# Performance work log

Hardware: AMD Instinct MI355X
Metric: run time of the kernel (lower is better)

Reference implementation:

```python
import jax, jax.numpy as jnp
import numpy as np

NUM_NEURONS = 256
NUM_SAMPLES = 512
MAX_SPIKES = 32
N_STEPS = 32          # fixed RK4 steps per spike round (stands in for adaptive Tsit5)
ALPHA = 0.03
V_RESET = 1.0
T0 = 0.0


def setup_inputs() -> dict:
    key = jax.random.key(0)
    ks = jax.random.split(key, 7)
    input_current = jax.random.normal(ks[0], (NUM_NEURONS,), dtype=jnp.float32)
    # _build_w with network=all-False: uniform(minval=0.5), mask sets nothing
    w = jax.random.uniform(ks[1], (NUM_NEURONS, NUM_NEURONS), minval=0.5, maxval=1.0, dtype=jnp.float32)
    mu = jax.random.uniform(ks[2], (2,), minval=0.5, maxval=1.0, dtype=jnp.float32)
    v0 = jax.random.normal(ks[3], (NUM_NEURONS,), dtype=jnp.float32)
    i0 = jax.random.normal(ks[4], (NUM_NEURONS,), dtype=jnp.float32)
    # s0 = log(U) - alpha  (always < 0)
    s0 = (jnp.log(jax.random.uniform(ks[5], (NUM_SAMPLES, NUM_NEURONS), minval=1e-6, maxval=1.0)) - ALPHA).astype(jnp.float32)
    # pre-drawn stochastic resets, one per (spike round, sample, neuron)
    reset_s = (jnp.log(jax.random.uniform(ks[6], (MAX_SPIKES, NUM_SAMPLES, NUM_NEURONS), minval=1e-6, maxval=1.0)) - ALPHA).astype(jnp.float32)
    return dict(input_current=input_current, w=w, mu=mu, v0=v0, i0=i0, s0=s0, reset_s=reset_s, t1=2)


def _drift(y, ic, mu1, mu2):
    # y: [samples, neurons, 3] = (v, i, s)
    v, i = y[..., 0], y[..., 1]
    dv = mu1 * (i + ic - v)
    di = -mu2 * i
    ds = jax.nn.sigmoid(v)  # intensity_fn(v)
    return jnp.stack([dv, di, ds], axis=-1)


def reference(input_current, w, mu, v0, i0, s0, reset_s, t1):
    t1f = jnp.float32(t1)
    mu1, mu2 = mu[0], mu[1]
    ic = input_current  # constant-in-time input current, [neurons]

    y0 = jnp.concatenate([
        jnp.broadcast_to(v0, (NUM_SAMPLES, NUM_NEURONS))[..., None],
        jnp.broadcast_to(i0, (NUM_SAMPLES, NUM_NEURONS))[..., None],
        s0[..., None]], axis=-1)  # [samples, neurons, 3]

    def rk4(y, h):
        k1 = _drift(y, ic, mu1, mu2)
        k2 = _drift(y + 0.5 * h * k1, ic, mu1, mu2)
        k3 = _drift(y + 0.5 * h * k2, ic, mu1, mu2)
        k4 = _drift(y + h * k3, ic, mu1, mu2)
        return y + (h / 6.0) * (k1 + 2.0 * k2 + 2.0 * k3 + k4)

    def round_body(carry, reset_k):
        t0s, y_in = carry                      # t0s: [samples]
        dt = (t1f - t0s) / N_STEPS             # per-sample step size
        h = dt[:, None, None]

        def step(sc, _):
            t, y, done, tev, yev, emask = sc
            y_new = rk4(y, h)
            y_new = jnp.where(done[:, None, None], y, y_new)  # freeze after event
            s_prev, s_new = y[..., 2], y_new[..., 2]
            crossed = s_new > 0.0                              # cond_fn root: s crosses 0
            trig = crossed.any(axis=1) & (~done)
            idx = jnp.argmax(s_new, axis=1)                    # event neuron (first/largest crossing)
            sp = jnp.take_along_axis(s_prev, idx[:, None], 1)[:, 0]
            sn = jnp.take_along_axis(s_new, idx[:, None], 1)[:, 0]
            frac = jnp.clip(sp / (sp - sn + 1e-12), 0.0, 1.0)  # linear root estimate (Newton stand-in)
            t_c = t + frac * dt
            y_c = y + frac[:, None, None] * (y_new - y)
            tev = jnp.where(trig, t_c, tev)
            yev = jnp.where(trig[:, None, None], y_c, yev)
            emask = jnp.where(trig[:, None], crossed, emask)
            y = jnp.where(trig[:, None, None], y_c, y_new)
            done = done | trig
            return (t + dt, y, done, tev, yev, emask), None

        done0 = jnp.zeros((NUM_SAMPLES,), bool)
        tev0 = jnp.full((NUM_SAMPLES,), jnp.inf, jnp.float32)
        em0 = jnp.zeros((NUM_SAMPLES, NUM_NEURONS), bool)
        (_, yend, done, tev, yev, emask), _ = jax.lax.scan(
            step, (t0s, y_in, done0, tev0, y_in, em0), None, length=N_STEPS)

        tev = jnp.where(done, tev, t1f)                 # no event -> sol.ts[-1] = t1
        yev = jnp.where(done[:, None, None], yev, yend)

        # trans_fn: spike reset + synaptic jump w[event_idx]
        eidx = jnp.argmax(emask, axis=1)
        w_row = jnp.where(done[:, None], w[eidx], 0.0)  # zero if no event happened
        v_t = yev[..., 0] - jnp.where(emask, V_RESET, 0.0)
        i_t = yev[..., 1] + w_row
        s_t = jnp.minimum(jnp.where(emask, reset_k, yev[..., 2]), 0.0)
        y_next = jnp.stack([v_t, i_t, s_t], axis=-1)
        return (tev, y_next), (tev, yev, emask)

    t0s = jnp.full((NUM_SAMPLES,), T0, jnp.float32)
    _, (tevs, yevs, emasks) = jax.lax.scan(jax.checkpoint(round_body), (t0s, y0), reset_s)

    spike_times = jnp.transpose(tevs, (1, 0))            # [samples, max_spikes]
    spike_values = jnp.transpose(yevs, (1, 0, 2, 3))     # [samples, max_spikes, neurons, 3]
    spike_marks = jnp.transpose(emasks, (1, 0, 2))       # [samples, max_spikes, neurons]
    return spike_times, spike_values, spike_marks
```

## Files before the change

kernel.cpp:

```cpp
#include <hip/hip_runtime.h>
#include <math.h>

#define NN 256
#define NS 512
#define MS 32
#define NSTEP 32
#define VRESET 1.0f

__device__ __forceinline__ float sigf(float x) {
    float e = __expf(-x);
    return __builtin_amdgcn_rcpf(1.0f + e);
}

__global__ __launch_bounds__(256) void snn_kernel(
    const float* __restrict__ ic_g,
    const float* __restrict__ w,
    const float* __restrict__ mu,
    const float* __restrict__ v0,
    const float* __restrict__ i0,
    const float* __restrict__ s0,
    const float* __restrict__ reset_s,
    const int*   __restrict__ t1p,
    float* __restrict__ out)
{
    const int tid  = threadIdx.x;
    const int lane = tid & 63;
    const int wid  = tid >> 6;
    const int samp = blockIdx.x;
    const double m1d = (double)mu[0];
    const double m2d = (double)mu[1];
    const float t1f = (float)t1p[0];

    __shared__ int   s_any[2][4];
    __shared__ float s_bv[4], s_bsp[4];
    __shared__ int   s_bn[4];
    __shared__ int   s_eidx[4];

    float v  = v0[tid];
    float ii = i0[tid];
    float s  = s0[samp * NN + tid];
    const float ic = ic_g[tid];
    float t0 = 0.0f;

    float* times = out;
    float* vals  = out + (size_t)NS * MS;
    float* marks = out + (size_t)NS * MS * (1 + NN * 3);

    for (int r = 0; r < MS; ++r) {
        const float dt = (t1f - t0) / (float)NSTEP;
        float tev = t1f;
        float yev_v, yev_i, yev_s;
        bool  em = false;
        bool  done = false;

        if (dt != 0.0f) {
            const double hd = (double)dt;
            const double a  = hd * m1d;
            const double b  = hd * m2d;
            const double p2 = 1.0 - 0.5 * a, q2 = 0.5 * a, r2 = 0.5 * a;
            const double i2c = 1.0 - 0.5 * b;
            const double p3 = 1.0 - 0.5 * a * p2;
            const double q3 = 0.5 * a * (i2c - q2);
            const double r3 = 0.5 * a * (1.0 - r2);
            const double i3c = 1.0 - 0.5 * b * i2c;
            const double p4 = 1.0 - a * p3;
            const double q4 = a * (i3c - q3);
            const double r4 = a * (1.0 - r3);
            const double i4c = 1.0 - b * i3c;
            const double a6 = a / 6.0, b6 = b / 6.0;
            const float fR00 = (float)(1.0 - a6 * (1.0 + 2.0 * p2 + 2.0 * p3 + p4));
            const float fR01 = (float)(a6 * (1.0 + 2.0 * (i2c - q2) + 2.0 * (i3c - q3) + (i4c - q4)));
            const float fC0  = (float)(a6 * (1.0 + 2.0 * (1.0 - r2) + 2.0 * (1.0 - r3) + (1.0 - r4)));
            const float fR11 = (float)(1.0 - b6 * (1.0 + 2.0 * i2c + 2.0 * i3c + i4c));
            const float fp2 = (float)p2, fq2 = (float)q2;
            const float fp3 = (float)p3, fq3 = (float)q3;
            const float fp4 = (float)p4, fq4 = (float)q4;
            const float r2ic = (float)r2 * ic;
            const float r3ic = (float)r3 * ic;
            const float r4ic = (float)r4 * ic;
            const float c0ic = fC0 * ic;
            const float h6 = dt * (1.0f / 6.0f);

            float t = t0, tprev = t0;
            float vp = v, ip = ii, sp = s;

            for (int st = 0; st <= NSTEP; ++st) {
                if (st > 0) {
                    int anyflag = s_any[(st - 1) & 1][0] | s_any[(st - 1) & 1][1] |
                                  s_any[(st - 1) & 1][2] | s_any[(st - 1) & 1][3];
                    if (anyflag) {
                        float bv = s, bsp = sp;
                        int   bn = tid;
#pragma unroll
                        for (int off = 32; off >= 1; off >>= 1) {
                            float ov  = __shfl_xor(bv, off);
                            float osp = __shfl_xor(bsp, off);
                            int   on  = __shfl_xor(bn, off);
                            if (ov > bv || (ov == bv && on < bn)) { bv = ov; bsp = osp; bn = on; }
                        }
                        if (lane == 0) { s_bv[wid] = bv; s_bsp[wid] = bsp; s_bn[wid] = bn; }
                        __syncthreads();
                        bv = s_bv[0]; bsp = s_bsp[0]; bn = s_bn[0];
#pragma unroll
                        for (int wv = 1; wv < 4; ++wv) {
                            float ov = s_bv[wv], osp = s_bsp[wv];
                            int   on = s_bn[wv];
                            if (ov > bv || (ov == bv && on < bn)) { bv = ov; bsp = osp; bn = on; }
                        }
                        float frac = bsp / (bsp - bv + 1e-12f);
                        frac = fminf(fmaxf(frac, 0.0f), 1.0f);
                        tev = tprev + frac * dt;
                        yev_v = vp + frac * (v  - vp);
                        yev_i = ip + frac * (ii - ip);
                        yev_s = sp + frac * (s  - sp);
                        em = s > 0.0f;
                        v = yev_v; ii = yev_i; s = yev_s;
                        done = true;
                        break;
                    }
                }
                if (st == NSTEP) break;

                vp = v; ip = ii; sp = s; tprev = t;
                float a2 = fmaf(fp2, vp, fmaf(fq2, ip, r2ic));
                float a3 = fmaf(fp3, vp, fmaf(fq3, ip, r3ic));
                float a4 = fmaf(fp4, vp, fmaf(fq4, ip, r4ic));
                float k1 = sigf(vp);
                float k2 = sigf(a2);
                float k3 = sigf(a3);
                float k4 = sigf(a4);
                v  = fmaf(fR00, vp, fmaf(fR01, ip, c0ic));
                ii = fR11 * ip;
                float ts = fmaf(2.0f, k2, k1);
                ts = fmaf(2.0f, k3, ts);
                ts = ts + k4;
                s = fmaf(h6, ts, sp);

                unsigned long long bl = __ballot(s > 0.0f);
                if (lane == 0) s_any[st & 1][wid] = (bl != 0ull) ? 1 : 0;
                t = tprev + dt;
                __syncthreads();
            }
        }

        if (!done) {
            tev = t1f;
            yev_v = v; yev_i = ii; yev_s = s; em = false;
        }

        const int sr = samp * MS + r;
        if (tid == 0) times[sr] = tev;
        {
            float* p = vals + ((size_t)sr * NN + tid) * 3;
            p[0] = yev_v;
            p[1] = yev_i;
            p[2] = yev_s;
            marks[(size_t)sr * NN + tid] = em ? 1.0f : 0.0f;
        }

        if (done) {
            unsigned long long bm = __ballot(em);
            int cand = (bm != 0ull) ? (wid * 64 + (int)__builtin_ctzll(bm)) : (2 * NN);
            if (lane == 0) s_eidx[wid] = cand;
            __syncthreads();
            int eidx = s_eidx[0];
            eidx = (s_eidx[1] < eidx) ? s_eidx[1] : eidx;
            eidx = (s_eidx[2] < eidx) ? s_eidx[2] : eidx;
            eidx = (s_eidx[3] < eidx) ? s_eidx[3] : eidx;

            float wr = w[eidx * NN + tid];
            v  = yev_v - (em ? VRESET : 0.0f);
            ii = yev_i + wr;
            float sres = em ? reset_s[((size_t)r * NS + samp) * NN + tid] : yev_s;
            s = fminf(sres, 0.0f);
        } else {
            s = fminf(s, 0.0f);
        }
        t0 = tev;
    }
}

extern "C" void kernel_launch(void* const* d_in, const int* in_sizes, int n_in,
                              void* d_out, int out_size, void* d_ws, size_t ws_size,
                              hipStream_t stream) {
    const float* ic      = (const float*)d_in[0];
    const float* w       = (const float*)d_in[1];
    const float* mu      = (const float*)d_in[2];
    const float* v0      = (const float*)d_in[3];
    const float* i0      = (const float*)d_in[4];
    const float* s0      = (const float*)d_in[5];
    const float* reset_s = (const float*)d_in[6];
    const int*   t1p     = (const int*)d_in[7];
    float* out = (float*)d_out;

    snn_kernel<<<dim3(NS), dim3(256), 0, stream>>>(ic, w, mu, v0, i0, s0,
                                                   reset_s, t1p, out);
}
```

Measured before the change: 158.1 us.

## Replace per-step block barriers with wave-local early exit and shared history

Removes the __syncthreads after every RK4 step. Each wave now integrates on its own, writes its s value per step into a shared history buffer, and on a local spike publishes the step via atomicMin and stops. Other waves poll the shared stop value. After a single barrier the block picks the earliest crossing step, reads s from history, and recomputes v and i by replaying the linear recurrence up to that step. The reset_s load is prefetched and the event-index reduction is merged into the argmax barrier. In exchange it adds about 33 KB of shared memory per block, which may cut occupancy, plus redundant replay work.

```diff
diff --git a/kernel.cpp b/kernel.cpp
--- a/kernel.cpp
+++ b/kernel.cpp
@@ -31,10 +31,10 @@
     const double m2d = (double)mu[1];
     const float t1f = (float)t1p[0];
 
-    __shared__ int   s_any[2][4];
+    __shared__ float s_hist[NSTEP + 1][NN];
+    __shared__ int   s_stop;
     __shared__ float s_bv[4], s_bsp[4];
-    __shared__ int   s_bn[4];
-    __shared__ int   s_eidx[4];
+    __shared__ int   s_bn[4], s_eidx[4];
 
     float v  = v0[tid];
     float ii = i0[tid];
@@ -52,6 +52,8 @@
         float yev_v, yev_i, yev_s;
         bool  em = false;
         bool  done = false;
+
+        const float rs_pref = reset_s[((size_t)r * NS + samp) * NN + tid];
 
         if (dt != 0.0f) {
             const double hd = (double)dt;
@@ -81,71 +83,102 @@
             const float c0ic = fC0 * ic;
             const float h6 = dt * (1.0f / 6.0f);
 
-            float t = t0, tprev = t0;
-            float vp = v, ip = ii, sp = s;
-
-            for (int st = 0; st <= NSTEP; ++st) {
-                if (st > 0) {
-                    int anyflag = s_any[(st - 1) & 1][0] | s_any[(st - 1) & 1][1] |
-                                  s_any[(st - 1) & 1][2] | s_any[(st - 1) & 1][3];
-                    if (anyflag) {
-                        float bv = s, bsp = sp;
-                        int   bn = tid;
-#pragma unroll
-                        for (int off = 32; off >= 1; off >>= 1) {
-                            float ov  = __shfl_xor(bv, off);
-                            float osp = __shfl_xor(bsp, off);
-                            int   on  = __shfl_xor(bn, off);
-                            if (ov > bv || (ov == bv && on < bn)) { bv = ov; bsp = osp; bn = on; }
-                        }
-                        if (lane == 0) { s_bv[wid] = bv; s_bsp[wid] = bsp; s_bn[wid] = bn; }
-                        __syncthreads();
-                        bv = s_bv[0]; bsp = s_bsp[0]; bn = s_bn[0];
-#pragma unroll
-                        for (int wv = 1; wv < 4; ++wv) {
-                            float ov = s_bv[wv], osp = s_bsp[wv];
-                            int   on = s_bn[wv];
-                            if (ov > bv || (ov == bv && on < bn)) { bv = ov; bsp = osp; bn = on; }
-                        }
-                        float frac = bsp / (bsp - bv + 1e-12f);
-                        frac = fminf(fmaxf(frac, 0.0f), 1.0f);
-                        tev = tprev + frac * dt;
-                        yev_v = vp + frac * (v  - vp);
-                        yev_i = ip + frac * (ii - ip);
-                        yev_s = sp + frac * (s  - sp);
-                        em = s > 0.0f;
-                        v = yev_v; ii = yev_i; s = yev_s;
-                        done = true;
-                        break;
-                    }
-                }
-                if (st == NSTEP) break;
-
-                vp = v; ip = ii; sp = s; tprev = t;
-                float a2 = fmaf(fp2, vp, fmaf(fq2, ip, r2ic));
-                float a3 = fmaf(fp3, vp, fmaf(fq3, ip, r3ic));
-                float a4 = fmaf(fp4, vp, fmaf(fq4, ip, r4ic));
-                float k1 = sigf(vp);
+            if (tid == 0) s_stop = NSTEP + 1;
+            s_hist[0][tid] = s;
+            __syncthreads();
+
+            float vv = v, iv = ii, sv = s;
+            int seen = NSTEP + 1;
+            for (int k = 1; k <= NSTEP; ++k) {
+                float a2 = fmaf(fp2, vv, fmaf(fq2, iv, r2ic));
+                float a3 = fmaf(fp3, vv, fmaf(fq3, iv, r3ic));
+                float a4 = fmaf(fp4, vv, fmaf(fq4, iv, r4ic));
+                float k1 = sigf(vv);
                 float k2 = sigf(a2);
                 float k3 = sigf(a3);
                 float k4 = sigf(a4);
-                v  = fmaf(fR00, vp, fmaf(fR01, ip, c0ic));
-                ii = fR11 * ip;
+                float vn  = fmaf(fR00, vv, fmaf(fR01, iv, c0ic));
+                float in_ = fR11 * iv;
                 float ts = fmaf(2.0f, k2, k1);
                 ts = fmaf(2.0f, k3, ts);
                 ts = ts + k4;
-                s = fmaf(h6, ts, sp);
-
-                unsigned long long bl = __ballot(s > 0.0f);
-                if (lane == 0) s_any[st & 1][wid] = (bl != 0ull) ? 1 : 0;
-                t = tprev + dt;
+                sv = fmaf(h6, ts, sv);
+                vv = vn; iv = in_;
+                s_hist[k][tid] = sv;
+                if (__any(sv > 0.0f)) {
+                    if (lane == 0) atomicMin(&s_stop, k);
+                    break;
+                }
+                if (seen <= k) break;
+                seen = *(volatile int*)&s_stop;
+            }
+            __syncthreads();
+            const int st = s_stop;
+
+            if (st <= NSTEP) {
+                float sn_ = s_hist[st][tid];
+                float sp_ = s_hist[st - 1][tid];
+                em = sn_ > 0.0f;
+
+                float bv = sn_, bsp = sp_;
+                int   bn = tid;
+#pragma unroll
+                for (int off = 32; off >= 1; off >>= 1) {
+                    float ov  = __shfl_xor(bv, off);
+                    float osp = __shfl_xor(bsp, off);
+                    int   on  = __shfl_xor(bn, off);
+                    if (ov > bv || (ov == bv && on < bn)) { bv = ov; bsp = osp; bn = on; }
+                }
+                unsigned long long bm = __ballot(em);
+                if (lane == 0) {
+                    s_bv[wid] = bv; s_bsp[wid] = bsp; s_bn[wid] = bn;
+                    s_eidx[wid] = (bm != 0ull) ? (wid * 64 + (int)__builtin_ctzll(bm))
+                                               : (2 * NN);
+                }
                 __syncthreads();
+                bv = s_bv[0]; bsp = s_bsp[0]; bn = s_bn[0];
+#pragma unroll
+                for (int wv = 1; wv < 4; ++wv) {
+                    float ov = s_bv[wv], osp = s_bsp[wv];
+                    int   on = s_bn[wv];
+                    if (ov > bv || (ov == bv && on < bn)) { bv = ov; bsp = osp; bn = on; }
+                }
+                int eidx = s_eidx[0];
+                eidx = (s_eidx[1] < eidx) ? s_eidx[1] : eidx;
+                eidx = (s_eidx[2] < eidx) ? s_eidx[2] : eidx;
+                eidx = (s_eidx[3] < eidx) ? s_eidx[3] : eidx;
+                float wr = w[eidx * NN + tid];
+
+                float frac = bsp / (bsp - bv + 1e-12f);
+                frac = fminf(fmaxf(frac, 0.0f), 1.0f);
+
+                float tprev = t0;
+                for (int q = 1; q < st; ++q) tprev += dt;
+                tev = tprev + frac * dt;
+
+                float rv = v, ri = ii;
+                for (int q = 1; q < st; ++q) {
+                    rv = fmaf(fR00, rv, fmaf(fR01, ri, c0ic));
+                    ri = fR11 * ri;
+                }
+                float vnew = fmaf(fR00, rv, fmaf(fR01, ri, c0ic));
+                float inew = fR11 * ri;
+                yev_v = rv + frac * (vnew - rv);
+                yev_i = ri + frac * (inew - ri);
+                yev_s = sp_ + frac * (sn_ - sp_);
+                done = true;
+
+                v  = yev_v - (em ? VRESET : 0.0f);
+                ii = yev_i + wr;
+                s  = fminf(em ? rs_pref : yev_s, 0.0f);
+            } else {
+                yev_v = vv; yev_i = iv; yev_s = sv;
+                v = vv; ii = iv;
+                s = fminf(sv, 0.0f);
             }
-        }
-
-        if (!done) {
-            tev = t1f;
-            yev_v = v; yev_i = ii; yev_s = s; em = false;
+        } else {
+            yev_v = v; yev_i = ii; yev_s = s;
+            s = fminf(s, 0.0f);
         }
 
         const int sr = samp * MS + r;
@@ -156,25 +189,6 @@
             p[1] = yev_i;
             p[2] = yev_s;
             marks[(size_t)sr * NN + tid] = em ? 1.0f : 0.0f;
-        }
-
-        if (done) {
-            unsigned long long bm = __ballot(em);
-            int cand = (bm != 0ull) ? (wid * 64 + (int)__builtin_ctzll(bm)) : (2 * NN);
-            if (lane == 0) s_eidx[wid] = cand;
-            __syncthreads();
-            int eidx = s_eidx[0];
-            eidx = (s_eidx[1] < eidx) ? s_eidx[1] : eidx;
-            eidx = (s_eidx[2] < eidx) ? s_eidx[2] : eidx;
-            eidx = (s_eidx[3] < eidx) ? s_eidx[3] : eidx;
-
-            float wr = w[eidx * NN + tid];
-            v  = yev_v - (em ? VRESET : 0.0f);
-            ii = yev_i + wr;
-            float sres = em ? reset_s[((size_t)r * NS + samp) * NN + tid] : yev_s;
-            s = fminf(sres, 0.0f);
-        } else {
-            s = fminf(s, 0.0f);
         }
         t0 = tev;
     }
```

New measurement: 155.9 us. No clear change (-1.4%).
